# Performance work log

Measured on AMD Instinct MI355X. Metric: run time of the kernel, lower is better.

Reference implementation:

```python
import jax, jax.numpy as jnp
import numpy as np

HIDDEN = 1024
HEADS = 16
CHUNK = 128
NEG_INF = -1e10  # matches source's -10000000000.0


def setup_inputs() -> dict:
    key = jax.random.key(0)
    k1, k2, k3 = jax.random.split(key, 3)
    B, S = 2, 4096
    x = jax.random.normal(k1, (B, S, HIDDEN), dtype=jnp.float32)
    w_qkv = jax.random.normal(k2, (HIDDEN, 3 * HIDDEN), dtype=jnp.float32) / np.sqrt(HIDDEN).astype(np.float32)
    w_out = jax.random.normal(k3, (HIDDEN, HIDDEN), dtype=jnp.float32) / np.sqrt(HIDDEN).astype(np.float32)
    return {"x": x, "w_qkv": w_qkv, "w_out": w_out}


def reference(x, w_qkv, w_out):
    B, S, _ = x.shape
    H, D = HEADS, HIDDEN // HEADS
    # fused qkv projection (flax Dense, no bias): [B,S,3,H,D]
    qkv = (x @ w_qkv).reshape(B, S, 3, H, D)
    q, k, v = qkv[:, :, 0], qkv[:, :, 1], qkv[:, :, 2]
    scale = jnp.sqrt(jnp.asarray(D, x.dtype))
    n_chunks = S // CHUNK
    # [n_chunks, B, CHUNK, H, D] query chunks; scan keeps only one chunk's
    # [B,H,CHUNK,S] score tensor live at a time (faithful to source's chunking).
    q_chunks = q.reshape(B, n_chunks, CHUNK, H, D).transpose(1, 0, 2, 3, 4)
    starts = jnp.arange(n_chunks) * CHUNK

    def step(carry, inp):
        qc, start = inp  # qc: [B,CHUNK,H,D]
        scores = jnp.einsum('bqhd,bkhd->bhqk', qc, k) / scale  # [B,H,CHUNK,S]
        causal = (jnp.arange(CHUNK)[:, None] + start) >= jnp.arange(S)[None, :]
        scores = jnp.where(causal[None, None], scores, NEG_INF)
        attn = jax.nn.softmax(scores, axis=-1)
        out_c = jnp.einsum('bhqk,bkhd->bqhd', attn, v).reshape(B, CHUNK, H * D)
        return carry, out_c

    _, outs = jax.lax.scan(step, None, (q_chunks, starts))  # [n,B,CHUNK,hidden]
    out = outs.transpose(1, 0, 2, 3).reshape(B, S, H * D)
    return out @ w_out
```

## Files before the change

kernel.cpp:

```cpp
#include <hip/hip_runtime.h>
#include <hip/hip_bf16.h>

#define SEQ 4096
#define BATCH 2
#define HEADS 16
#define DHEAD 64
#define HID 1024

typedef unsigned short ushort_t;
typedef __attribute__((ext_vector_type(8))) short short8;
typedef __attribute__((ext_vector_type(4))) float f32x4;

__device__ __forceinline__ float exp2_fast(float x) {
  return __builtin_amdgcn_exp2f(x);
}

__device__ __forceinline__ ushort_t f2b(float f) {
  unsigned u = __builtin_bit_cast(unsigned, f);
  unsigned r = 0x7fffu + ((u >> 16) & 1u);
  return (ushort_t)((u + r) >> 16);
}

__device__ __forceinline__ unsigned cvt_pk_bf16(float lo, float hi) {
  unsigned r;
  asm("v_cvt_pk_bf16_f32 %0, %1, %2" : "=v"(r) : "v"(lo), "v"(hi));
  return r;
}

__device__ __forceinline__ void gload16(const void* g, void* l) {
  __builtin_amdgcn_global_load_lds((const __attribute__((address_space(1))) void*)g,
                                   (__attribute__((address_space(3))) void*)l, 16, 0, 0);
}

__device__ __forceinline__ f32x4 mfma_bf16(short8 a, short8 b, f32x4 c) {
  return __builtin_amdgcn_mfma_f32_16x16x32_bf16(a, b, c, 0, 0, 0);
}

__global__ void cvt_kernel(const float* __restrict__ in, ushort_t* __restrict__ out, int n4) {
  int i = blockIdx.x * blockDim.x + threadIdx.x;
  if (i >= n4) return;
  float4 v = reinterpret_cast<const float4*>(in)[i];
  ushort4 o;
  o.x = f2b(v.x); o.y = f2b(v.y); o.z = f2b(v.z); o.w = f2b(v.w);
  reinterpret_cast<ushort4*>(out)[i] = o;
}

__global__ void transpose_cvt_kernel(const float* __restrict__ in, ushort_t* __restrict__ out,
                                     int rows, int cols) {
  __shared__ float tile[32][33];
  int tx = threadIdx.x & 31, ty = threadIdx.x >> 5;
  int r0 = blockIdx.y * 32, c0 = blockIdx.x * 32;
#pragma unroll
  for (int i = 0; i < 32; i += 8)
    tile[ty + i][tx] = in[(size_t)(r0 + ty + i) * cols + c0 + tx];
  __syncthreads();
#pragma unroll
  for (int i = 0; i < 32; i += 8)
    out[(size_t)(c0 + ty + i) * rows + r0 + tx] = f2b(tile[tx][ty + i]);
}

template <int MODE>
__global__ __launch_bounds__(256, 2)
void gemm_kernel(const ushort_t* __restrict__ A, const ushort_t* __restrict__ BT,
                 int M, int N, int K,
                 ushort_t* __restrict__ qg, ushort_t* __restrict__ kg,
                 ushort_t* __restrict__ vTg, float* __restrict__ outf) {
  __shared__ ushort_t lA[128 * 64];
  __shared__ ushort_t lB[128 * 64];
  int tid = threadIdx.x;
  int lane = tid & 63, w = tid >> 6;
  int m0 = blockIdx.x * 128, n0 = blockIdx.y * 128;
  int wr = (w >> 1) * 64, wc = (w & 1) * 64;
  int lr = lane & 15, lg = lane >> 4;

  const f32x4 z4 = {0.f, 0.f, 0.f, 0.f};
  f32x4 acc[4][4];
#pragma unroll
  for (int m = 0; m < 4; ++m)
#pragma unroll
    for (int n = 0; n < 4; ++n) acc[m][n] = z4;

  int ktiles = K >> 6;
  for (int kt = 0; kt < ktiles; ++kt) {
    int k0 = kt << 6;
#pragma unroll
    for (int i = 0; i < 4; ++i) {
      int c = i * 256 + tid;
      int row = c >> 3, cc = c & 7;
      gload16(A + (size_t)(m0 + row) * K + k0 + (cc ^ (row & 7)) * 8, lA + c * 8);
    }
#pragma unroll
    for (int i = 0; i < 4; ++i) {
      int c = i * 256 + tid;
      int row = c >> 3, cc = c & 7;
      gload16(BT + (size_t)(n0 + row) * K + k0 + (cc ^ (row & 7)) * 8, lB + c * 8);
    }
    __syncthreads();
#pragma unroll
    for (int kk = 0; kk < 2; ++kk) {
      short8 a[4], b[4];
#pragma unroll
      for (int m = 0; m < 4; ++m) {
        int row = wr + m * 16 + lr, cc = kk * 4 + lg;
        a[m] = *(const short8*)(lA + row * 64 + ((cc ^ (row & 7)) << 3));
      }
#pragma unroll
      for (int n = 0; n < 4; ++n) {
        int row = wc + n * 16 + lr, cc = kk * 4 + lg;
        b[n] = *(const short8*)(lB + row * 64 + ((cc ^ (row & 7)) << 3));
      }
      __builtin_amdgcn_s_setprio(1);
#pragma unroll
      for (int m = 0; m < 4; ++m)
#pragma unroll
        for (int n = 0; n < 4; ++n)
          acc[m][n] = mfma_bf16(a[m], b[n], acc[m][n]);
      __builtin_amdgcn_s_setprio(0);
    }
    __syncthreads();
  }

#pragma unroll
  for (int m = 0; m < 4; ++m)
#pragma unroll
    for (int n = 0; n < 4; ++n)
#pragma unroll
      for (int r = 0; r < 4; ++r) {
        int i = m0 + wr + m * 16 + lg * 4 + r;
        int j = n0 + wc + n * 16 + lr;
        float v = acc[m][n][r];
        if (MODE == 0) {
          int mat = j >> 10, rem = j & 1023;
          int h = rem >> 6, d = rem & 63;
          int b = i >> 12, s = i & 4095;
          int bh = b * HEADS + h;
          ushort_t val = f2b(mat == 0 ? v * 0.18033688f : v);
          if (mat == 0)      qg[((size_t)bh * SEQ + s) * DHEAD + d] = val;
          else if (mat == 1) kg[((size_t)bh * SEQ + s) * DHEAD + d] = val;
          else               vTg[((size_t)bh * DHEAD + d) * SEQ + s] = val;
        } else {
          outf[(size_t)i * N + j] = v;
        }
      }
}

struct QState {
  short8 qf[2][2];
  float mrow[2], lsum[2];
  f32x4 o[2][4];
};

__device__ __forceinline__ void attn_tile(int jt, int qt, int w, int lr, int lg, int lane,
                                          const ushort_t* lKc, const ushort_t* lVc,
                                          ushort_t* lP, QState& st) {
  const f32x4 z4 = {0.f, 0.f, 0.f, 0.f};
  f32x4 s[2][8];
#pragma unroll
  for (int qm = 0; qm < 2; ++qm)
#pragma unroll
    for (int kt = 0; kt < 8; ++kt) s[qm][kt] = z4;
#pragma unroll
  for (int kk = 0; kk < 2; ++kk) {
#pragma unroll
    for (int kt = 0; kt < 8; ++kt) {
      int row = kt * 16 + lr;
      short8 kf = *(const short8*)(lKc + row * 64 + (((kk * 4 + lg) ^ (row & 7)) << 3));
      __builtin_amdgcn_s_setprio(1);
      s[0][kt] = mfma_bf16(kf, st.qf[0][kk], s[0][kt]);
      s[1][kt] = mfma_bf16(kf, st.qf[1][kk], s[1][kt]);
      __builtin_amdgcn_s_setprio(0);
    }
  }

  if (jt == qt) {
#pragma unroll
    for (int qm = 0; qm < 2; ++qm) {
      int qgl = w * 32 + qm * 16 + lr;
#pragma unroll
      for (int kt = 0; kt < 8; ++kt)
#pragma unroll
        for (int r = 0; r < 4; ++r)
          if (kt * 16 + lg * 4 + r > qgl) s[qm][kt][r] = -1e30f;
    }
  }

  int slot = w * 16 + lr;
#pragma unroll
  for (int qm = 0; qm < 2; ++qm) {
    float mx = s[qm][0][0];
#pragma unroll
    for (int kt = 0; kt < 8; ++kt)
#pragma unroll
      for (int r = 0; r < 4; ++r) mx = fmaxf(mx, s[qm][kt][r]);
    mx = fmaxf(mx, __shfl_xor(mx, 16));
    mx = fmaxf(mx, __shfl_xor(mx, 32));
    float mo = st.mrow[qm];
    if (!__all(mx - mo <= 8.0f)) {
      float mn = fmaxf(mo, mx);
      float al = exp2_fast(mo - mn);
      st.mrow[qm] = mn;
      st.lsum[qm] *= al;
#pragma unroll
      for (int r = 0; r < 4; ++r) {
        float alo = __shfl(al, (lane & 48) | (lg * 4 + r));
#pragma unroll
        for (int nd = 0; nd < 4; ++nd) st.o[qm][nd][r] *= alo;
      }
    }
    float mloc = st.mrow[qm];
    float rs = 0.f;
#pragma unroll
    for (int kt = 0; kt < 8; ++kt)
#pragma unroll
      for (int r = 0; r < 4; ++r) {
        float p = exp2_fast(s[qm][kt][r] - mloc);
        s[qm][kt][r] = p;
        rs += p;
      }
    rs += __shfl_xor(rs, 16);
    rs += __shfl_xor(rs, 32);
    st.lsum[qm] += rs;

#pragma unroll
    for (int kt = 0; kt < 8; ++kt) {
      uint2 pw;
      pw.x = cvt_pk_bf16(s[qm][kt][0], s[qm][kt][1]);
      pw.y = cvt_pk_bf16(s[qm][kt][2], s[qm][kt][3]);
      int c = kt * 2 + (lg >> 1);
      *(uint2*)(lP + slot * 128 + (((c ^ lr) << 3) | ((lg & 1) << 2))) = pw;
    }

#pragma unroll
    for (int kk = 0; kk < 4; ++kk) {
      short8 a = *(const short8*)(lP + slot * 128 + (((kk * 4 + lg) ^ lr) << 3));
#pragma unroll
      for (int nd = 0; nd < 4; ++nd) {
        int row = nd * 16 + lr;
        short8 b = *(const short8*)(lVc + row * 128 + (((kk * 4 + lg) ^ (row & 15)) << 3));
        __builtin_amdgcn_s_setprio(1);
        st.o[qm][nd] = mfma_bf16(a, b, st.o[qm][nd]);
        __builtin_amdgcn_s_setprio(0);
      }
    }
  }
}

__device__ __forceinline__ void attn_epilogue(const QState& st, int q0, int bh,
                                              int w, int lr, int lg, int lane,
                                              ushort_t* __restrict__ og) {
  int b = bh >> 4, h = bh & 15;
#pragma unroll
  for (int m = 0; m < 2; ++m)
#pragma unroll
    for (int r = 0; r < 4; ++r) {
      float ls = __shfl(st.lsum[m], (lane & 48) | (lg * 4 + r));
      float inv = 1.0f / ls;
      int srow = q0 + w * 32 + m * 16 + lg * 4 + r;
#pragma unroll
      for (int nd = 0; nd < 4; ++nd) {
        int col = h * 64 + nd * 16 + lr;
        og[((size_t)b * SEQ + srow) * HID + col] = f2b(st.o[m][nd][r] * inv);
      }
    }
}

__global__ __launch_bounds__(256, 2)
void attn_kernel(const ushort_t* __restrict__ qg, const ushort_t* __restrict__ kg,
                 const ushort_t* __restrict__ vTg, ushort_t* __restrict__ og) {
  __shared__ ushort_t lK[2][128 * 64];
  __shared__ ushort_t lV[2][64 * 128];
  __shared__ ushort_t lP[64 * 128];

  int bid = blockIdx.x;
  int wg = (bid & 7) * 64 + (bid >> 3);
  int bh = wg >> 4;
  int pair = wg & 15;
  int qtA = 31 - pair, qtB = pair;
  int q0A = qtA * 128, q0B = qtB * 128;
  const ushort_t* Q = qg + (size_t)bh * SEQ * DHEAD;
  const ushort_t* Kp = kg + (size_t)bh * SEQ * DHEAD;
  const ushort_t* Vt = vTg + (size_t)bh * DHEAD * SEQ;

  int tid = threadIdx.x, lane = tid & 63, w = tid >> 6;
  int lr = lane & 15, lg = lane >> 4;

#pragma unroll
  for (int i = 0; i < 4; ++i) {
    int c = i * 256 + tid;
    int row = c >> 3, cc = c & 7;
    size_t qoff = (cc ^ (row & 7)) * 8;
    gload16(Q + (size_t)(q0A + row) * DHEAD + qoff, &lK[1][c * 8]);
    gload16(Q + (size_t)(q0B + row) * DHEAD + qoff, &lV[1][c * 8]);
    gload16(Kp + (size_t)row * DHEAD + qoff, &lK[0][c * 8]);
  }
#pragma unroll
  for (int i = 0; i < 4; ++i) {
    int c = i * 256 + tid;
    int d = c >> 4, cc = c & 15;
    gload16(Vt + (size_t)d * SEQ + (cc ^ (d & 15)) * 8, &lV[0][c * 8]);
  }
  __syncthreads();

  QState stA, stB;
#pragma unroll
  for (int qm = 0; qm < 2; ++qm)
#pragma unroll
    for (int kk = 0; kk < 2; ++kk) {
      int row = w * 32 + qm * 16 + lr;
      int off = row * 64 + (((kk * 4 + lg) ^ (row & 7)) << 3);
      stA.qf[qm][kk] = *(const short8*)(&lK[1][0] + off);
      stB.qf[qm][kk] = *(const short8*)(&lV[1][0] + off);
    }
  asm volatile("s_waitcnt lgkmcnt(0)");
  __syncthreads();

  const f32x4 z4 = {0.f, 0.f, 0.f, 0.f};
#pragma unroll
  for (int qm = 0; qm < 2; ++qm) {
    stA.mrow[qm] = -1e30f; stA.lsum[qm] = 0.f;
    stB.mrow[qm] = -1e30f; stB.lsum[qm] = 0.f;
#pragma unroll
    for (int n = 0; n < 4; ++n) { stA.o[qm][n] = z4; stB.o[qm][n] = z4; }
  }

  for (int jt = 0; jt <= qtA; ++jt) {
    int cur = jt & 1, nxt = cur ^ 1;
    if (jt < qtA) {
      int j0n = (jt + 1) * 128;
#pragma unroll
      for (int i = 0; i < 4; ++i) {
        int c = i * 256 + tid;
        int row = c >> 3, cc = c & 7;
        gload16(Kp + (size_t)(j0n + row) * DHEAD + (cc ^ (row & 7)) * 8, &lK[nxt][c * 8]);
      }
#pragma unroll
      for (int i = 0; i < 4; ++i) {
        int c = i * 256 + tid;
        int d = c >> 4, cc = c & 15;
        gload16(Vt + (size_t)d * SEQ + j0n + (cc ^ (d & 15)) * 8, &lV[nxt][c * 8]);
      }
    }

    attn_tile(jt, qtA, w, lr, lg, lane, &lK[cur][0], &lV[cur][0], lP, stA);
    if (jt <= qtB) attn_tile(jt, qtB, w, lr, lg, lane, &lK[cur][0], &lV[cur][0], lP, stB);

    __syncthreads();
  }

  attn_epilogue(stA, q0A, bh, w, lr, lg, lane, og);
  attn_epilogue(stB, q0B, bh, w, lr, lg, lane, og);
}

extern "C" void kernel_launch(void* const* d_in, const int* in_sizes, int n_in,
                              void* d_out, int out_size, void* d_ws, size_t ws_size,
                              hipStream_t stream) {
  const float* x = (const float*)d_in[0];
  const float* wqkv = (const float*)d_in[1];
  const float* wout = (const float*)d_in[2];
  float* out = (float*)d_out;

  if (ws_size < 75497472u) return;

  char* ws = (char*)d_ws;
  ushort_t* xb    = (ushort_t*)(ws);
  ushort_t* wqkvT = (ushort_t*)(ws + 16777216);
  ushort_t* woutT = (ushort_t*)(ws + 23068672);
  ushort_t* qgb   = (ushort_t*)(ws + 25165824);
  ushort_t* kgb   = (ushort_t*)(ws + 41943040);
  ushort_t* vTb   = (ushort_t*)(ws + 58720256);
  ushort_t* ob    = xb;

  cvt_kernel<<<dim3(8192), dim3(256), 0, stream>>>(x, xb, 2097152);
  transpose_cvt_kernel<<<dim3(96, 32), dim3(256), 0, stream>>>(wqkv, wqkvT, 1024, 3072);
  transpose_cvt_kernel<<<dim3(32, 32), dim3(256), 0, stream>>>(wout, woutT, 1024, 1024);
  gemm_kernel<0><<<dim3(64, 24), dim3(256), 0, stream>>>(xb, wqkvT, 8192, 3072, 1024,
                                                         qgb, kgb, vTb, nullptr);
  attn_kernel<<<dim3(512), dim3(256), 0, stream>>>(qgb, kgb, vTb, ob);
  gemm_kernel<1><<<dim3(64, 8), dim3(256), 0, stream>>>(ob, woutT, 8192, 1024, 1024,
                                                        nullptr, nullptr, nullptr, out);
}
```

Baseline: 240.8 us.

## Switch attention to 32x32x16 MFMA and keep P in registers via permlane swap

Rewrites the attention tile to use 32x32x16 bf16 MFMA instead of 16x16x32, with each wave owning 32 query rows as one tile. The softmax probabilities are converted to bf16 and rearranged across lanes with v_permlane32_swap so they feed the PV MFMA straight from registers, which removes the LDS round trip through the lP buffer and its shared memory footprint. This cuts LDS traffic and instruction count per tile. The cost is more accumulator registers per wave (f32x16 tiles), which may raise register pressure under the 2-blocks-per-CU launch bound.

```diff
diff --git a/kernel.cpp b/kernel.cpp
--- a/kernel.cpp
+++ b/kernel.cpp
@@ -8,8 +8,11 @@
 #define HID 1024
 
 typedef unsigned short ushort_t;
+typedef unsigned int uint_t;
 typedef __attribute__((ext_vector_type(8))) short short8;
 typedef __attribute__((ext_vector_type(4))) float f32x4;
+typedef __attribute__((ext_vector_type(16))) float f32x16;
+typedef __attribute__((ext_vector_type(4))) uint_t u32x4;
 
 __device__ __forceinline__ float exp2_fast(float x) {
   return __builtin_amdgcn_exp2f(x);
@@ -21,10 +24,14 @@
   return (ushort_t)((u + r) >> 16);
 }
 
-__device__ __forceinline__ unsigned cvt_pk_bf16(float lo, float hi) {
-  unsigned r;
+__device__ __forceinline__ uint_t cvt_pk_bf16(float lo, float hi) {
+  uint_t r;
   asm("v_cvt_pk_bf16_f32 %0, %1, %2" : "=v"(r) : "v"(lo), "v"(hi));
   return r;
+}
+
+__device__ __forceinline__ void permlane_swap(uint_t& a, uint_t& b) {
+  asm("v_permlane32_swap_b32 %0, %1" : "+v"(a), "+v"(b));
 }
 
 __device__ __forceinline__ void gload16(const void* g, void* l) {
@@ -34,6 +41,10 @@
 
 __device__ __forceinline__ f32x4 mfma_bf16(short8 a, short8 b, f32x4 c) {
   return __builtin_amdgcn_mfma_f32_16x16x32_bf16(a, b, c, 0, 0, 0);
+}
+
+__device__ __forceinline__ f32x16 mfma32_bf16(short8 a, short8 b, f32x16 c) {
+  return __builtin_amdgcn_mfma_f32_32x32x16_bf16(a, b, c, 0, 0, 0);
 }
 
 __global__ void cvt_kernel(const float* __restrict__ in, ushort_t* __restrict__ out, int n4) {
@@ -144,124 +155,125 @@
       }
 }
 
-struct QState {
-  short8 qf[2][2];
-  float mrow[2], lsum[2];
-  f32x4 o[2][4];
+struct QS {
+  short8 qf[4];
+  f32x16 o[2];
+  float mrow, lsum;
 };
 
-__device__ __forceinline__ void attn_tile(int jt, int qt, int w, int lr, int lg, int lane,
-                                          const ushort_t* lKc, const ushort_t* lVc,
-                                          ushort_t* lP, QState& st) {
-  const f32x4 z4 = {0.f, 0.f, 0.f, 0.f};
-  f32x4 s[2][8];
-#pragma unroll
-  for (int qm = 0; qm < 2; ++qm)
-#pragma unroll
-    for (int kt = 0; kt < 8; ++kt) s[qm][kt] = z4;
-#pragma unroll
-  for (int kk = 0; kk < 2; ++kk) {
-#pragma unroll
-    for (int kt = 0; kt < 8; ++kt) {
-      int row = kt * 16 + lr;
-      short8 kf = *(const short8*)(lKc + row * 64 + (((kk * 4 + lg) ^ (row & 7)) << 3));
+__device__ __forceinline__ void attn_tile(int diag, int w, int l31, int hi, int lane,
+                                          const ushort_t* lKc, const ushort_t* lVc, QS& st) {
+  f32x16 s[4];
+#pragma unroll
+  for (int t = 0; t < 4; ++t)
+#pragma unroll
+    for (int r = 0; r < 16; ++r) s[t][r] = 0.f;
+
+#pragma unroll
+  for (int t = 0; t < 4; ++t) {
+    int row = t * 32 + l31;
+#pragma unroll
+    for (int kb = 0; kb < 4; ++kb) {
+      int cc = kb * 2 + hi;
+      short8 kf = *(const short8*)(lKc + row * 64 + ((cc ^ (row & 7)) << 3));
       __builtin_amdgcn_s_setprio(1);
-      s[0][kt] = mfma_bf16(kf, st.qf[0][kk], s[0][kt]);
-      s[1][kt] = mfma_bf16(kf, st.qf[1][kk], s[1][kt]);
+      s[t] = mfma32_bf16(kf, st.qf[kb], s[t]);
       __builtin_amdgcn_s_setprio(0);
     }
   }
 
-  if (jt == qt) {
-#pragma unroll
-    for (int qm = 0; qm < 2; ++qm) {
-      int qgl = w * 32 + qm * 16 + lr;
-#pragma unroll
-      for (int kt = 0; kt < 8; ++kt)
-#pragma unroll
-        for (int r = 0; r < 4; ++r)
-          if (kt * 16 + lg * 4 + r > qgl) s[qm][kt][r] = -1e30f;
-    }
-  }
-
-  int slot = w * 16 + lr;
-#pragma unroll
-  for (int qm = 0; qm < 2; ++qm) {
-    float mx = s[qm][0][0];
-#pragma unroll
-    for (int kt = 0; kt < 8; ++kt)
-#pragma unroll
-      for (int r = 0; r < 4; ++r) mx = fmaxf(mx, s[qm][kt][r]);
-    mx = fmaxf(mx, __shfl_xor(mx, 16));
-    mx = fmaxf(mx, __shfl_xor(mx, 32));
-    float mo = st.mrow[qm];
-    if (!__all(mx - mo <= 8.0f)) {
-      float mn = fmaxf(mo, mx);
-      float al = exp2_fast(mo - mn);
-      st.mrow[qm] = mn;
-      st.lsum[qm] *= al;
-#pragma unroll
-      for (int r = 0; r < 4; ++r) {
-        float alo = __shfl(al, (lane & 48) | (lg * 4 + r));
-#pragma unroll
-        for (int nd = 0; nd < 4; ++nd) st.o[qm][nd][r] *= alo;
-      }
-    }
-    float mloc = st.mrow[qm];
-    float rs = 0.f;
-#pragma unroll
-    for (int kt = 0; kt < 8; ++kt)
-#pragma unroll
-      for (int r = 0; r < 4; ++r) {
-        float p = exp2_fast(s[qm][kt][r] - mloc);
-        s[qm][kt][r] = p;
-        rs += p;
-      }
-    rs += __shfl_xor(rs, 16);
-    rs += __shfl_xor(rs, 32);
-    st.lsum[qm] += rs;
-
-#pragma unroll
-    for (int kt = 0; kt < 8; ++kt) {
-      uint2 pw;
-      pw.x = cvt_pk_bf16(s[qm][kt][0], s[qm][kt][1]);
-      pw.y = cvt_pk_bf16(s[qm][kt][2], s[qm][kt][3]);
-      int c = kt * 2 + (lg >> 1);
-      *(uint2*)(lP + slot * 128 + (((c ^ lr) << 3) | ((lg & 1) << 2))) = pw;
-    }
-
-#pragma unroll
-    for (int kk = 0; kk < 4; ++kk) {
-      short8 a = *(const short8*)(lP + slot * 128 + (((kk * 4 + lg) ^ lr) << 3));
-#pragma unroll
-      for (int nd = 0; nd < 4; ++nd) {
-        int row = nd * 16 + lr;
-        short8 b = *(const short8*)(lVc + row * 128 + (((kk * 4 + lg) ^ (row & 15)) << 3));
-        __builtin_amdgcn_s_setprio(1);
-        st.o[qm][nd] = mfma_bf16(a, b, st.o[qm][nd]);
-        __builtin_amdgcn_s_setprio(0);
-      }
-    }
-  }
-}
-
-__device__ __forceinline__ void attn_epilogue(const QState& st, int q0, int bh,
-                                              int w, int lr, int lg, int lane,
+  if (diag) {
+    int q = w * 32 + l31;
+#pragma unroll
+    for (int t = 0; t < 4; ++t)
+#pragma unroll
+      for (int r = 0; r < 16; ++r)
+        if (t * 32 + (r & 3) + 8 * (r >> 2) + 4 * hi > q) s[t][r] = -1e30f;
+  }
+
+  float mx = s[0][0];
+#pragma unroll
+  for (int t = 0; t < 4; ++t)
+#pragma unroll
+    for (int r = 0; r < 16; ++r) mx = fmaxf(mx, s[t][r]);
+  mx = fmaxf(mx, __shfl_xor(mx, 32));
+  float mo = st.mrow;
+  if (!__all(mx - mo <= 8.0f)) {
+    float mn = fmaxf(mo, mx);
+    float al = exp2_fast(mo - mn);
+    st.mrow = mn;
+    st.lsum *= al;
+#pragma unroll
+    for (int r = 0; r < 16; ++r) {
+      float alo = __shfl(al, (r & 3) + 8 * (r >> 2) + 4 * hi);
+      st.o[0][r] *= alo;
+      st.o[1][r] *= alo;
+    }
+  }
+  float mloc = st.mrow;
+  float rs = 0.f;
+#pragma unroll
+  for (int t = 0; t < 4; ++t)
+#pragma unroll
+    for (int r = 0; r < 16; ++r) {
+      float p = exp2_fast(s[t][r] - mloc);
+      s[t][r] = p;
+      rs += p;
+    }
+  rs += __shfl_xor(rs, 32);
+  st.lsum += rs;
+
+  short8 pa[8];
+#pragma unroll
+  for (int t = 0; t < 4; ++t) {
+    uint_t w0 = cvt_pk_bf16(s[t][0], s[t][1]);
+    uint_t w1 = cvt_pk_bf16(s[t][2], s[t][3]);
+    uint_t w2 = cvt_pk_bf16(s[t][4], s[t][5]);
+    uint_t w3 = cvt_pk_bf16(s[t][6], s[t][7]);
+    permlane_swap(w0, w2);
+    permlane_swap(w1, w3);
+    u32x4 f0 = {w0, w1, w2, w3};
+    pa[2 * t] = __builtin_bit_cast(short8, f0);
+    uint_t w4 = cvt_pk_bf16(s[t][8], s[t][9]);
+    uint_t w5 = cvt_pk_bf16(s[t][10], s[t][11]);
+    uint_t w6 = cvt_pk_bf16(s[t][12], s[t][13]);
+    uint_t w7 = cvt_pk_bf16(s[t][14], s[t][15]);
+    permlane_swap(w4, w6);
+    permlane_swap(w5, w7);
+    u32x4 f1 = {w4, w5, w6, w7};
+    pa[2 * t + 1] = __builtin_bit_cast(short8, f1);
+  }
+
+#pragma unroll
+  for (int nd = 0; nd < 2; ++nd) {
+    int row = nd * 32 + l31;
+#pragma unroll
+    for (int kb = 0; kb < 8; ++kb) {
+      int cc = kb * 2 + hi;
+      short8 vf = *(const short8*)(lVc + row * 128 + ((cc ^ (row & 15)) << 3));
+      __builtin_amdgcn_s_setprio(1);
+      st.o[nd] = mfma32_bf16(pa[kb], vf, st.o[nd]);
+      __builtin_amdgcn_s_setprio(0);
+    }
+  }
+}
+
+__device__ __forceinline__ void attn_epilogue(const QS& st, int q0, int bh,
+                                              int w, int l31, int hi,
                                               ushort_t* __restrict__ og) {
   int b = bh >> 4, h = bh & 15;
 #pragma unroll
-  for (int m = 0; m < 2; ++m)
-#pragma unroll
-    for (int r = 0; r < 4; ++r) {
-      float ls = __shfl(st.lsum[m], (lane & 48) | (lg * 4 + r));
-      float inv = 1.0f / ls;
-      int srow = q0 + w * 32 + m * 16 + lg * 4 + r;
-#pragma unroll
-      for (int nd = 0; nd < 4; ++nd) {
-        int col = h * 64 + nd * 16 + lr;
-        og[((size_t)b * SEQ + srow) * HID + col] = f2b(st.o[m][nd][r] * inv);
-      }
-    }
+  for (int r = 0; r < 16; ++r) {
+    int qr = (r & 3) + 8 * (r >> 2) + 4 * hi;
+    float ls = __shfl(st.lsum, qr);
+    float inv = 1.0f / ls;
+    int srow = q0 + w * 32 + qr;
+#pragma unroll
+    for (int nd = 0; nd < 2; ++nd) {
+      int col = h * 64 + nd * 32 + l31;
+      og[((size_t)b * SEQ + srow) * HID + col] = f2b(st.o[nd][r] * inv);
+    }
+  }
 }
 
 __global__ __launch_bounds__(256, 2)
@@ -269,7 +281,6 @@
                  const ushort_t* __restrict__ vTg, ushort_t* __restrict__ og) {
   __shared__ ushort_t lK[2][128 * 64];
   __shared__ ushort_t lV[2][64 * 128];
-  __shared__ ushort_t lP[64 * 128];
 
   int bid = blockIdx.x;
   int wg = (bid & 7) * 64 + (bid >> 3);
@@ -282,7 +293,7 @@
   const ushort_t* Vt = vTg + (size_t)bh * DHEAD * SEQ;
 
   int tid = threadIdx.x, lane = tid & 63, w = tid >> 6;
-  int lr = lane & 15, lg = lane >> 4;
+  int l31 = lane & 31, hi = lane >> 5;
 
 #pragma unroll
   for (int i = 0; i < 4; ++i) {
@@ -301,27 +312,24 @@
   }
   __syncthreads();
 
-  QState stA, stB;
-#pragma unroll
-  for (int qm = 0; qm < 2; ++qm)
-#pragma unroll
-    for (int kk = 0; kk < 2; ++kk) {
-      int row = w * 32 + qm * 16 + lr;
-      int off = row * 64 + (((kk * 4 + lg) ^ (row & 7)) << 3);
-      stA.qf[qm][kk] = *(const short8*)(&lK[1][0] + off);
-      stB.qf[qm][kk] = *(const short8*)(&lV[1][0] + off);
-    }
+  QS stA, stB;
+  int qrow = w * 32 + l31;
+#pragma unroll
+  for (int kb = 0; kb < 4; ++kb) {
+    int cc = kb * 2 + hi;
+    int off = qrow * 64 + ((cc ^ (qrow & 7)) << 3);
+    stA.qf[kb] = *(const short8*)(&lK[1][0] + off);
+    stB.qf[kb] = *(const short8*)(&lV[1][0] + off);
+  }
   asm volatile("s_waitcnt lgkmcnt(0)");
   __syncthreads();
 
-  const f32x4 z4 = {0.f, 0.f, 0.f, 0.f};
-#pragma unroll
-  for (int qm = 0; qm < 2; ++qm) {
-    stA.mrow[qm] = -1e30f; stA.lsum[qm] = 0.f;
-    stB.mrow[qm] = -1e30f; stB.lsum[qm] = 0.f;
-#pragma unroll
-    for (int n = 0; n < 4; ++n) { stA.o[qm][n] = z4; stB.o[qm][n] = z4; }
-  }
+  stA.mrow = -1e30f; stA.lsum = 0.f;
+  stB.mrow = -1e30f; stB.lsum = 0.f;
+#pragma unroll
+  for (int nd = 0; nd < 2; ++nd)
+#pragma unroll
+    for (int r = 0; r < 16; ++r) { stA.o[nd][r] = 0.f; stB.o[nd][r] = 0.f; }
 
   for (int jt = 0; jt <= qtA; ++jt) {
     int cur = jt & 1, nxt = cur ^ 1;
@@ -341,14 +349,15 @@
       }
     }
 
-    attn_tile(jt, qtA, w, lr, lg, lane, &lK[cur][0], &lV[cur][0], lP, stA);
-    if (jt <= qtB) attn_tile(jt, qtB, w, lr, lg, lane, &lK[cur][0], &lV[cur][0], lP, stB);
+    attn_tile(jt == qtA, w, l31, hi, lane, &lK[cur][0], &lV[cur][0], stA);
+    if (jt <= qtB)
+      attn_tile(jt == qtB, w, l31, hi, lane, &lK[cur][0], &lV[cur][0], stB);
 
     __syncthreads();
   }
 
-  attn_epilogue(stA, q0A, bh, w, lr, lg, lane, og);
-  attn_epilogue(stB, q0B, bh, w, lr, lg, lane, og);
+  attn_epilogue(stA, q0A, bh, w, l31, hi, og);
+  attn_epilogue(stB, q0B, bh, w, l31, hi, og);
 }
 
 extern "C" void kernel_launch(void* const* d_in, const int* in_sizes, int n_in,
```

Measured after the change: 218.1 us. -9.4%, faster.
